# Kernel tuning notes

Measured on AMD Instinct MI355X. Metric: run time of the kernel, lower is better.

The kernel has to match this reference:

```python
import jax, jax.numpy as jnp
import numpy as np

B, T, O, N, M, H = 64, 128, 256, 65536, 64, 512
EPS = 1e-8


def setup_inputs() -> dict:
    key = jax.random.key(0)
    ks = jax.random.split(key, 8)
    x = jax.random.normal(ks[0], (B, T, O, 1), dtype=jnp.float32)
    # original: memory.uniform_(1e-05, 0.0001)
    memory0 = jax.random.uniform(ks[1], (N, M), dtype=jnp.float32, minval=1e-5, maxval=1e-4)
    eye = jnp.eye(B, N, dtype=jnp.float32)  # torch.eye(batch_size, N)
    h0 = jnp.zeros((B, H), dtype=jnp.float32)
    Wxh = jax.random.normal(ks[2], (O, H), dtype=jnp.float32) * 0.05
    Wrh = jax.random.normal(ks[3], (M, H), dtype=jnp.float32) * 0.1
    bh = jnp.zeros((H,), dtype=jnp.float32)
    Wo = jax.random.normal(ks[4], (H, O), dtype=jnp.float32) * 0.05
    bo = jnp.zeros((O,), dtype=jnp.float32)
    rW = jax.random.normal(ks[5], (H, M + 6), dtype=jnp.float32) * 0.05
    rb = jnp.zeros((M + 6,), dtype=jnp.float32)
    wW = jax.random.normal(ks[6], (H, 3 * M + 6), dtype=jnp.float32) * 0.05
    wb = jnp.zeros((3 * M + 6,), dtype=jnp.float32)
    return dict(x=x, memory0=memory0, wr=eye, ww=eye, h0=h0, Wxh=Wxh, Wrh=Wrh,
                bh=bh, Wo=Wo, bo=bo, rW=rW, rb=rb, wW=wW, wb=wb)


def _address(head_out, w_prev, mem):
    """Graves-2014 NTM addressing. head_out: (B, M+6) raw head projection."""
    k = jnp.tanh(head_out[:, :M])                          # key       (B, M)
    beta = jax.nn.softplus(head_out[:, M:M + 1])           # strength  (B, 1)
    g = jax.nn.sigmoid(head_out[:, M + 1:M + 2])           # gate      (B, 1)
    s = jax.nn.softmax(head_out[:, M + 2:M + 5], axis=-1)  # shift     (B, 3)
    gamma = 1.0 + jax.nn.softplus(head_out[:, M + 5:M + 6])  # sharpen (B, 1)
    kn = k / (jnp.linalg.norm(k, axis=-1, keepdims=True) + EPS)
    mn = mem / (jnp.linalg.norm(mem, axis=-1, keepdims=True) + EPS)
    wc = jax.nn.softmax(beta * (kn @ mn.T), axis=-1)       # content   (B, N)
    wg = g * wc + (1.0 - g) * w_prev                       # interpolate
    # circular shift conv over N with taps {-1, 0, +1}
    wt = (s[:, 0:1] * jnp.roll(wg, 1, axis=1)
          + s[:, 1:2] * wg
          + s[:, 2:3] * jnp.roll(wg, -1, axis=1))
    wp = (wt + EPS) ** gamma                               # sharpen
    return wp / jnp.sum(wp, axis=1, keepdims=True)


def reference(x, memory0, wr, ww, h0, Wxh, Wrh, bh, Wo, bo, rW, rb, wW, wb):
    xt = jnp.transpose(x, (1, 0, 2, 3)).reshape(T, B, O)  # time-major, flattened
    inv_b = 1.0 / B

    def step(carry, x_t):
        mem, h = carry
        # write head: address, then erase/add (memory shared across batch -> mean)
        wh = h @ wW + wb                                   # (B, 3M+6)
        w_w = _address(wh[:, :M + 6], ww, mem)             # (B, N)
        e = jax.nn.sigmoid(wh[:, M + 6:2 * M + 6])         # (B, M)
        a = jnp.tanh(wh[:, 2 * M + 6:3 * M + 6])           # (B, M)
        erase = jnp.einsum('bn,bm->nm', w_w, e) * inv_b    # (N, M)
        add = jnp.einsum('bn,bm->nm', w_w, a) * inv_b
        m_t = mem * (1.0 - erase) + add
        # read head
        rh = h @ rW + rb                                   # (B, M+6)
        w_r = _address(rh, wr, m_t)                        # (B, N)
        r_t = w_r @ m_t                                    # (B, M)
        # feedforward controller step + output
        h_new = jax.nn.relu(x_t @ Wxh + r_t @ Wrh + bh)    # (B, H)
        out = jax.nn.sigmoid(h_new @ Wo + bo)              # (B, O)
        return (m_t, h_new), out

    (_, _), outs = jax.lax.scan(step, (memory0, h0), xt)   # outs: (T, B, O)
    return jnp.transpose(outs, (1, 0, 2))                  # (B, T, O)
```

## Files before the change

### kernel.cpp

```cpp
#include <hip/hip_runtime.h>

#define NROWS 65536
#define BB 64
#define TT 128
#define OO 256
#define MM 64
#define HH 512
#define EPSF 1e-8f

__device__ __forceinline__ float wredsum(float v) {
#pragma unroll
  for (int o = 1; o < 64; o <<= 1) v += __shfl_xor(v, o, 64);
  return v;
}
__device__ __forceinline__ float sigm(float x) { return 1.f / (1.f + __expf(-x)); }
__device__ __forceinline__ float softplus_(float x) { return x > 20.f ? x : log1pf(__expf(x)); }

__global__ void __launch_bounds__(256) k_xpre(const float* __restrict__ x, const float* __restrict__ Wxh,
                                              const float* __restrict__ bh, float* __restrict__ Xpre) {
  __shared__ float xl[4][256];
  int tid = threadIdx.x;
#pragma unroll
  for (int i = 0; i < 4; ++i) {
    int pair = blockIdx.x * 4 + i;
    int t = pair >> 6, b = pair & 63;
    xl[i][tid] = x[((size_t)b * TT + t) * OO + tid];
  }
  __syncthreads();
  for (int u = 0; u < 2; ++u) {
    int hh = tid + u * 256;
    float a[4];
    float bv = bh[hh];
#pragma unroll
    for (int i = 0; i < 4; ++i) a[i] = bv;
    for (int o = 0; o < 256; ++o) {
      float wv = Wxh[(size_t)o * HH + hh];
#pragma unroll
      for (int i = 0; i < 4; ++i) a[i] += xl[i][o] * wv;
    }
#pragma unroll
    for (int i = 0; i < 4; ++i) {
      int pair = blockIdx.x * 4 + i;
      Xpre[(size_t)pair * HH + hh] = a[i];
    }
  }
}

__global__ void __launch_bounds__(256) k_w1(const float* __restrict__ msrc, const float* __restrict__ knwT,
                                            const float* __restrict__ prmw, float* __restrict__ E,
                                            float* __restrict__ Swst, float* __restrict__ S2rst) {
  int tid = threadIdx.x, blk = blockIdx.x;
  int base = blk * 64;
  __shared__ float rows[4096];
  __shared__ float sred[256];
  if (blk == 0) {
    for (int i = tid; i < 32 * 64; i += 256) S2rst[i] = 0.f;
  }
  {
    const float4* s4 = (const float4*)(msrc + (size_t)base * 64);
    float4* d4 = (float4*)rows;
#pragma unroll
    for (int i = 0; i < 4; ++i) d4[tid + i * 256] = s4[tid + i * 256];
  }
  int l = tid & 63, w = tid >> 6;
  float kr[64];
#pragma unroll
  for (int j = 0; j < 64; ++j) kr[j] = knwT[j * 64 + l];
  float beta = prmw[l * 8 + 0];
  __syncthreads();
  float sacc = 0.f;
  for (int r = w * 16; r < w * 16 + 16; ++r) {
    const float4* row4 = (const float4*)(rows + r * 64);
    float dot = 0.f, nsq = 0.f;
#pragma unroll
    for (int j = 0; j < 16; ++j) {
      float4 rv = row4[j];
      dot += kr[j * 4] * rv.x + kr[j * 4 + 1] * rv.y + kr[j * 4 + 2] * rv.z + kr[j * 4 + 3] * rv.w;
      nsq += rv.x * rv.x + rv.y * rv.y + rv.z * rv.z + rv.w * rv.w;
    }
    float ev = __expf(beta * dot / (sqrtf(nsq) + EPSF) - beta);
    E[(size_t)(base + r) * 64 + l] = ev;
    sacc += ev;
  }
  sred[tid] = sacc;
  __syncthreads();
  if (tid < 64)
    atomicAdd(&Swst[(blk & 31) * 64 + tid], sred[tid] + sred[tid + 64] + sred[tid + 128] + sred[tid + 192]);
}

__global__ void __launch_bounds__(256) k_w2(const float* __restrict__ E, const float* __restrict__ prmw,
                                            const float* __restrict__ Swst, float* __restrict__ wpg,
                                            float* __restrict__ S2wst) {
  int tid = threadIdx.x, blk = blockIdx.x, base = blk * 64;
  __shared__ float EL[66 * 64];
  __shared__ float Sw[64];
  __shared__ float sred[256];
  if (tid < 64) {
    float s = 0.f;
    for (int st = 0; st < 32; ++st) s += Swst[st * 64 + tid];
    Sw[tid] = s;
  }
  for (int i = tid; i < 66 * 64; i += 256) {
    int rr = i >> 6, b2 = i & 63;
    EL[i] = E[(size_t)((base - 1 + rr) & (NROWS - 1)) * 64 + b2];
  }
  __syncthreads();
  int b = tid & 63, w = tid >> 6;
  float g = prmw[b * 8 + 1], gam = prmw[b * 8 + 2];
  float s0 = prmw[b * 8 + 3], s1 = prmw[b * 8 + 4], s2 = prmw[b * 8 + 5];
  float gi = g / Sw[b], gm1 = 1.f - g;
  float s2acc = 0.f;
  for (int i = 0; i < 16; ++i) {
    int ln = w + i * 4;
    int n = base + ln;
    int nm = (n - 1) & (NROWS - 1), np = (n + 1) & (NROWS - 1);
    float wgm = gi * EL[ln * 64 + b] + (nm == b ? gm1 : 0.f);
    float wgc = gi * EL[(ln + 1) * 64 + b] + (n == b ? gm1 : 0.f);
    float wgp = gi * EL[(ln + 2) * 64 + b] + (np == b ? gm1 : 0.f);
    float wt = s0 * wgm + s1 * wgc + s2 * wgp;
    float wp = __powf(wt + EPSF, gam);
    wpg[(size_t)n * 64 + b] = wp;
    s2acc += wp;
  }
  sred[tid] = s2acc;
  __syncthreads();
  if (tid < 64)
    atomicAdd(&S2wst[(blk & 31) * 64 + tid], sred[tid] + sred[tid + 64] + sred[tid + 128] + sred[tid + 192]);
}

__global__ void __launch_bounds__(256) k_w3(const float* __restrict__ msrc, float* __restrict__ mdst,
                                            const float* __restrict__ wpg, const float* __restrict__ ea2,
                                            const float* __restrict__ knrT, const float* __restrict__ prmr,
                                            const float* __restrict__ S2wst, float* __restrict__ E,
                                            float* __restrict__ Srst) {
  int tid = threadIdx.x, blk = blockIdx.x, base = blk * 64;
  __shared__ float2 ealds[4096];
  __shared__ float wlT[4 * 64 * 20];
  __shared__ float fb[64];
  __shared__ float sred[256];
  {
    const float4* s4 = (const float4*)ea2;
    float4* d4 = (float4*)ealds;
#pragma unroll
    for (int i = 0; i < 8; ++i) d4[tid + i * 256] = s4[tid + i * 256];
  }
  if (tid < 64) {
    float s = 0.f;
    for (int st = 0; st < 32; ++st) s += S2wst[st * 64 + tid];
    fb[tid] = 1.f / (64.f * s);
  }
  __syncthreads();
  int l = tid & 63, w = tid >> 6;
#pragma unroll
  for (int k = 0; k < 16; ++k) {
    float wv = wpg[(size_t)(base + w * 16 + k) * 64 + l] * fb[l];
    wlT[(w * 64 + l) * 20 + k] = wv;
  }
  __syncthreads();
  float er[16], ad[16];
#pragma unroll
  for (int k = 0; k < 16; ++k) { er[k] = 0.f; ad[k] = 0.f; }
  for (int b2 = 0; b2 < 64; ++b2) {
    float2 eav = ealds[b2 * 64 + l];
    const float4* wrow = (const float4*)(wlT + (w * 64 + b2) * 20);
    float4 q0 = wrow[0], q1 = wrow[1], q2 = wrow[2], q3 = wrow[3];
    float qa[16];
    qa[0] = q0.x; qa[1] = q0.y; qa[2] = q0.z; qa[3] = q0.w;
    qa[4] = q1.x; qa[5] = q1.y; qa[6] = q1.z; qa[7] = q1.w;
    qa[8] = q2.x; qa[9] = q2.y; qa[10] = q2.z; qa[11] = q2.w;
    qa[12] = q3.x; qa[13] = q3.y; qa[14] = q3.z; qa[15] = q3.w;
#pragma unroll
    for (int k = 0; k < 16; ++k) { er[k] += qa[k] * eav.x; ad[k] += qa[k] * eav.y; }
  }
#pragma unroll
  for (int k = 0; k < 16; ++k) {
    int r = w * 16 + k;
    size_t n = (size_t)(base + r);
    float mv = msrc[n * 64 + l];
    mdst[n * 64 + l] = mv * (1.f - er[k]) + ad[k];
  }
  __syncthreads();
  float kr[64];
#pragma unroll
  for (int j = 0; j < 64; ++j) kr[j] = knrT[j * 64 + l];
  float beta_r = prmr[l * 8 + 0];
  float sacc = 0.f;
  for (int r = w * 16; r < w * 16 + 16; ++r) {
    const float4* row4 = (const float4*)(mdst + (size_t)(base + r) * 64);
    float dot = 0.f, nsq = 0.f;
#pragma unroll
    for (int j = 0; j < 16; ++j) {
      float4 rv = row4[j];
      dot += kr[j * 4] * rv.x + kr[j * 4 + 1] * rv.y + kr[j * 4 + 2] * rv.z + kr[j * 4 + 3] * rv.w;
      nsq += rv.x * rv.x + rv.y * rv.y + rv.z * rv.z + rv.w * rv.w;
    }
    float ev = __expf(beta_r * dot / (sqrtf(nsq) + EPSF) - beta_r);
    E[(size_t)(base + r) * 64 + l] = ev;
    sacc += ev;
  }
  sred[tid] = sacc;
  __syncthreads();
  if (tid < 64)
    atomicAdd(&Srst[(blk & 31) * 64 + tid], sred[tid] + sred[tid + 64] + sred[tid + 128] + sred[tid + 192]);
}

__global__ void __launch_bounds__(256) k_r2(const float* __restrict__ E, const float* __restrict__ mdst,
                                            const float* __restrict__ prmr, const float* __restrict__ Srst,
                                            float* __restrict__ part, float* __restrict__ S2rst) {
  int tid = threadIdx.x, blk = blockIdx.x, base = blk * 64;
  __shared__ float mt[4096];
  __shared__ float EL[66 * 64];
  __shared__ float Sr[64];
  __shared__ float sred[256];
  __shared__ float racc[64 * 65];
  if (tid < 64) {
    float s = 0.f;
    for (int st = 0; st < 32; ++st) s += Srst[st * 64 + tid];
    Sr[tid] = s;
  }
  {
    const float4* s4 = (const float4*)(mdst + (size_t)base * 64);
    float4* d4 = (float4*)mt;
#pragma unroll
    for (int i = 0; i < 4; ++i) d4[tid + i * 256] = s4[tid + i * 256];
  }
  for (int i = tid; i < 66 * 64; i += 256) {
    int rr = i >> 6, b2 = i & 63;
    EL[i] = E[(size_t)((base - 1 + rr) & (NROWS - 1)) * 64 + b2];
  }
  __syncthreads();
  int b = tid & 63, w = tid >> 6;
  float g = prmr[b * 8 + 1], gam = prmr[b * 8 + 2];
  float s0 = prmr[b * 8 + 3], s1 = prmr[b * 8 + 4], s2 = prmr[b * 8 + 5];
  float gi = g / Sr[b], gm1 = 1.f - g;
  float acc[64];
#pragma unroll
  for (int m = 0; m < 64; ++m) acc[m] = 0.f;
  float s2acc = 0.f;
  for (int i = 0; i < 16; ++i) {
    int r = w * 16 + i;
    int n = base + r;
    int nm = (n - 1) & (NROWS - 1), np = (n + 1) & (NROWS - 1);
    float wgm = gi * EL[r * 64 + b] + (nm == b ? gm1 : 0.f);
    float wgc = gi * EL[(r + 1) * 64 + b] + (n == b ? gm1 : 0.f);
    float wgp = gi * EL[(r + 2) * 64 + b] + (np == b ? gm1 : 0.f);
    float wt = s0 * wgm + s1 * wgc + s2 * wgp;
    float wp = __powf(wt + EPSF, gam);
    s2acc += wp;
    const float4* row4 = (const float4*)(mt + r * 64);
#pragma unroll
    for (int m4 = 0; m4 < 16; ++m4) {
      float4 mv = row4[m4];
      acc[m4 * 4 + 0] += wp * mv.x;
      acc[m4 * 4 + 1] += wp * mv.y;
      acc[m4 * 4 + 2] += wp * mv.z;
      acc[m4 * 4 + 3] += wp * mv.w;
    }
  }
  sred[tid] = s2acc;
  __syncthreads();
  if (tid < 64)
    atomicAdd(&S2rst[(blk & 31) * 64 + tid], sred[tid] + sred[tid + 64] + sred[tid + 128] + sred[tid + 192]);
  if (w == 0) {
#pragma unroll
    for (int m = 0; m < 64; ++m) racc[b * 65 + m] = acc[m];
  }
  __syncthreads();
  for (int ww2 = 1; ww2 < 4; ++ww2) {
    if (w == ww2) {
#pragma unroll
      for (int m = 0; m < 64; ++m) racc[b * 65 + m] += acc[m];
    }
    __syncthreads();
  }
  for (int i = tid; i < 4096; i += 256) part[(size_t)blk * 4096 + i] = racc[(i >> 6) * 65 + (i & 63)];
}

__global__ void __launch_bounds__(256) k_rr(const float* __restrict__ part, float* __restrict__ part2) {
  __shared__ float red[256];
  int rb = blockIdx.x;
  int b = rb >> 2, quarter = rb & 3;
  int tid = threadIdx.x;
  int m = tid & 63, pq = tid >> 6;
  float acc = 0.f;
  for (int p = quarter * 256 + pq; p < quarter * 256 + 256; p += 4)
    acc += part[((size_t)p * 64 + b) * 64 + m];
  red[tid] = acc;
  __syncthreads();
  if (tid < 64)
    part2[(size_t)rb * 64 + tid] = red[tid] + red[tid + 64] + red[tid + 128] + red[tid + 192];
}

__global__ void __launch_bounds__(512) k_cp(int t, const float* __restrict__ h0,
                                            const float* __restrict__ Xpre, float* __restrict__ Hbuf,
                                            const float* __restrict__ part2, const float* __restrict__ S2rst,
                                            const float* __restrict__ Wrh, const float* __restrict__ wW,
                                            const float* __restrict__ wb, const float* __restrict__ rW,
                                            const float* __restrict__ rb, float* __restrict__ knwT,
                                            float* __restrict__ knrT, float* __restrict__ ea2,
                                            float* __restrict__ prmw, float* __restrict__ prmr,
                                            float* __restrict__ zst) {
  int b = blockIdx.x, tid = threadIdx.x;
  __shared__ float hl[512];
  __shared__ float proj[268];
  __shared__ float red[512];
  __shared__ float rt[64];
  __shared__ float s2r_sh;
  if (t >= 0) {
    float v = 0.f;
    if (tid < 32) v = S2rst[tid * 64 + b];
    if (tid < 64) red[tid] = v;
    __syncthreads();
    if (tid == 0) {
      float s = 0.f;
      for (int i = 0; i < 32; ++i) s += red[i];
      s2r_sh = s;
    }
    __syncthreads();
    if (tid < 256) {
      int m = tid & 63, q = tid >> 6;
      red[tid] = part2[((size_t)b * 4 + q) * 64 + m];
    }
    __syncthreads();
    if (tid < 64) rt[tid] = (red[tid] + red[tid + 64] + red[tid + 128] + red[tid + 192]) / s2r_sh;
    __syncthreads();
    {
      int hh = tid;
      float a = Xpre[((size_t)t * 64 + b) * HH + hh];
      for (int m2 = 0; m2 < 64; ++m2) a += rt[m2] * Wrh[(size_t)m2 * HH + hh];
      a = fmaxf(a, 0.f);
      Hbuf[((size_t)t * 64 + b) * HH + hh] = a;
      hl[hh] = a;
    }
  } else {
    hl[tid] = h0[(size_t)b * HH + tid];
  }
  __syncthreads();
  if (b == 0) {
    for (int i = tid; i < 3 * 2048; i += 512) zst[i] = 0.f;
  }
  if (tid < 268) {
    int idx = tid;
    float a;
    if (idx < 198) {
      a = wb[idx];
      for (int hh = 0; hh < 512; ++hh) a += hl[hh] * wW[(size_t)hh * 198 + idx];
    } else {
      int jj = idx - 198;
      a = rb[jj];
      for (int hh = 0; hh < 512; ++hh) a += hl[hh] * rW[(size_t)hh * 70 + jj];
    }
    proj[idx] = a;
  }
  __syncthreads();
  int l = tid & 63, wv = tid >> 6;
  if (wv == 0) {
    float kv = tanhf(proj[l]);
    float s = wredsum(kv * kv);
    knwT[l * 64 + b] = kv / (sqrtf(s) + EPSF);
  } else if (wv == 1) {
    float kv = tanhf(proj[198 + l]);
    float s = wredsum(kv * kv);
    knrT[l * 64 + b] = kv / (sqrtf(s) + EPSF);
  } else if (wv == 2) {
    float ev = sigm(proj[70 + l]);
    float av = tanhf(proj[134 + l]);
    ((float2*)ea2)[b * 64 + l] = make_float2(ev, av);
  } else if (wv == 3) {
    if (l == 0) {
      float beta = softplus_(proj[64]);
      float g = sigm(proj[65]);
      float v0 = proj[66], v1 = proj[67], v2 = proj[68];
      float mx = fmaxf(v0, fmaxf(v1, v2));
      float e0 = __expf(v0 - mx), e1 = __expf(v1 - mx), e2 = __expf(v2 - mx);
      float is = 1.f / (e0 + e1 + e2);
      float gam = 1.f + softplus_(proj[69]);
      prmw[b * 8 + 0] = beta; prmw[b * 8 + 1] = g; prmw[b * 8 + 2] = gam;
      prmw[b * 8 + 3] = e0 * is; prmw[b * 8 + 4] = e1 * is; prmw[b * 8 + 5] = e2 * is;
    } else if (l == 1) {
      const int of = 198;
      float beta = softplus_(proj[of + 64]);
      float g = sigm(proj[of + 65]);
      float v0 = proj[of + 66], v1 = proj[of + 67], v2 = proj[of + 68];
      float mx = fmaxf(v0, fmaxf(v1, v2));
      float e0 = __expf(v0 - mx), e1 = __expf(v1 - mx), e2 = __expf(v2 - mx);
      float is = 1.f / (e0 + e1 + e2);
      float gam = 1.f + softplus_(proj[of + 69]);
      prmr[b * 8 + 0] = beta; prmr[b * 8 + 1] = g; prmr[b * 8 + 2] = gam;
      prmr[b * 8 + 3] = e0 * is; prmr[b * 8 + 4] = e1 * is; prmr[b * 8 + 5] = e2 * is;
    }
  }
}

__global__ void __launch_bounds__(256) k_out(const float* __restrict__ Hbuf, const float* __restrict__ Wo,
                                             const float* __restrict__ bo, float* __restrict__ out) {
  __shared__ float hl[4][512];
  int tid = threadIdx.x;
#pragma unroll
  for (int i = 0; i < 8; ++i) {
    int idx = tid + i * 256;
    hl[idx >> 9][idx & 511] = Hbuf[(size_t)blockIdx.x * 2048 + idx];
  }
  __syncthreads();
  float a[4];
  float bv = bo[tid];
#pragma unroll
  for (int i = 0; i < 4; ++i) a[i] = bv;
  for (int hh = 0; hh < 512; ++hh) {
    float wv = Wo[(size_t)hh * OO + tid];
#pragma unroll
    for (int i = 0; i < 4; ++i) a[i] += hl[i][hh] * wv;
  }
#pragma unroll
  for (int i = 0; i < 4; ++i) {
    int pair = blockIdx.x * 4 + i;
    int t = pair >> 6, b = pair & 63;
    out[((size_t)b * TT + t) * OO + tid] = 1.f / (1.f + __expf(-a[i]));
  }
}

extern "C" void kernel_launch(void* const* d_in, const int* in_sizes, int n_in,
                              void* d_out, int out_size, void* d_ws, size_t ws_size,
                              hipStream_t stream) {
  (void)in_sizes; (void)n_in; (void)out_size; (void)ws_size;
  const float* x    = (const float*)d_in[0];
  const float* mem0 = (const float*)d_in[1];
  const float* h0   = (const float*)d_in[4];
  const float* Wxh  = (const float*)d_in[5];
  const float* Wrh  = (const float*)d_in[6];
  const float* bh   = (const float*)d_in[7];
  const float* Wo   = (const float*)d_in[8];
  const float* bo   = (const float*)d_in[9];
  const float* rW   = (const float*)d_in[10];
  const float* rb   = (const float*)d_in[11];
  const float* wW   = (const float*)d_in[12];
  const float* wb   = (const float*)d_in[13];
  float* ws = (float*)d_ws;
  const size_t NM = (size_t)NROWS * MM;
  float* memA = ws;
  float* memB = memA + NM;
  float* E    = memB + NM;
  float* wpg  = E + NM;
  float* Xpre = wpg + NM;
  float* Hbuf = Xpre + NM;
  float* part = Hbuf + NM;
  float* part2 = part + NM;
  float* small = part2 + 16384;
  float* knwT = small;
  float* knrT = knwT + 4096;
  float* ea2  = knrT + 4096;
  float* prmw = ea2 + 8192;
  float* prmr = prmw + 512;
  float* Swst  = prmr + 512;
  float* S2wst = Swst + 2048;
  float* Srst  = S2wst + 2048;
  float* S2rst = Srst + 2048;

  hipMemcpyAsync(memA, mem0, NM * sizeof(float), hipMemcpyDeviceToDevice, stream);
  k_xpre<<<2048, 256, 0, stream>>>(x, Wxh, bh, Xpre);
  k_cp<<<64, 512, 0, stream>>>(-1, h0, Xpre, Hbuf, part2, S2rst, Wrh, wW, wb, rW, rb,
                               knwT, knrT, ea2, prmw, prmr, Swst);
  for (int t = 0; t < TT; ++t) {
    float* msrc = (t & 1) ? memB : memA;
    float* mdst = (t & 1) ? memA : memB;
    k_w1<<<1024, 256, 0, stream>>>(msrc, knwT, prmw, E, Swst, S2rst);
    k_w2<<<1024, 256, 0, stream>>>(E, prmw, Swst, wpg, S2wst);
    k_w3<<<1024, 256, 0, stream>>>(msrc, mdst, wpg, ea2, knrT, prmr, S2wst, E, Srst);
    k_r2<<<1024, 256, 0, stream>>>(E, mdst, prmr, Srst, part, S2rst);
    k_rr<<<256, 256, 0, stream>>>(part, part2);
    k_cp<<<64, 512, 0, stream>>>(t, h0, Xpre, Hbuf, part2, S2rst, Wrh, wW, wb, rW, rb,
                                 knwT, knrT, ea2, prmw, prmr, Swst);
  }
  k_out<<<2048, 256, 0, stream>>>(Hbuf, Wo, bo, (float*)d_out);
}
```

Measured before the change: 27.03 ms.

## Cache updated memory rows in LDS and fold partial read reduction into controller kernel

The write-update kernel stores each updated memory row in shared memory as well as global memory. The read-addressing similarity pass then reads from LDS instead of reloading from global. The separate partial-sum reduction kernel is removed, and the controller kernel now reduces all 1024 per-block partials itself, saving one launch per timestep and the intermediate buffer. The trade-off is a larger LDS footprint in k_w3 and a much larger serial reduction in the 64-block controller kernel.

```diff
diff --git a/kernel.cpp b/kernel.cpp
--- a/kernel.cpp
+++ b/kernel.cpp
@@ -136,6 +136,7 @@
   int tid = threadIdx.x, blk = blockIdx.x, base = blk * 64;
   __shared__ float2 ealds[4096];
   __shared__ float wlT[4 * 64 * 20];
+  __shared__ float rowsN[4096];
   __shared__ float fb[64];
   __shared__ float sred[256];
   {
@@ -177,7 +178,9 @@
     int r = w * 16 + k;
     size_t n = (size_t)(base + r);
     float mv = msrc[n * 64 + l];
-    mdst[n * 64 + l] = mv * (1.f - er[k]) + ad[k];
+    float nv = mv * (1.f - er[k]) + ad[k];
+    mdst[n * 64 + l] = nv;
+    rowsN[r * 64 + l] = nv;
   }
   __syncthreads();
   float kr[64];
@@ -186,7 +189,7 @@
   float beta_r = prmr[l * 8 + 0];
   float sacc = 0.f;
   for (int r = w * 16; r < w * 16 + 16; ++r) {
-    const float4* row4 = (const float4*)(mdst + (size_t)(base + r) * 64);
+    const float4* row4 = (const float4*)(rowsN + r * 64);
     float dot = 0.f, nsq = 0.f;
 #pragma unroll
     for (int j = 0; j < 16; ++j) {
@@ -276,24 +279,9 @@
   for (int i = tid; i < 4096; i += 256) part[(size_t)blk * 4096 + i] = racc[(i >> 6) * 65 + (i & 63)];
 }
 
-__global__ void __launch_bounds__(256) k_rr(const float* __restrict__ part, float* __restrict__ part2) {
-  __shared__ float red[256];
-  int rb = blockIdx.x;
-  int b = rb >> 2, quarter = rb & 3;
-  int tid = threadIdx.x;
-  int m = tid & 63, pq = tid >> 6;
-  float acc = 0.f;
-  for (int p = quarter * 256 + pq; p < quarter * 256 + 256; p += 4)
-    acc += part[((size_t)p * 64 + b) * 64 + m];
-  red[tid] = acc;
-  __syncthreads();
-  if (tid < 64)
-    part2[(size_t)rb * 64 + tid] = red[tid] + red[tid + 64] + red[tid + 128] + red[tid + 192];
-}
-
 __global__ void __launch_bounds__(512) k_cp(int t, const float* __restrict__ h0,
                                             const float* __restrict__ Xpre, float* __restrict__ Hbuf,
-                                            const float* __restrict__ part2, const float* __restrict__ S2rst,
+                                            const float* __restrict__ part, const float* __restrict__ S2rst,
                                             const float* __restrict__ Wrh, const float* __restrict__ wW,
                                             const float* __restrict__ wb, const float* __restrict__ rW,
                                             const float* __restrict__ rb, float* __restrict__ knwT,
@@ -317,12 +305,19 @@
       s2r_sh = s;
     }
     __syncthreads();
-    if (tid < 256) {
+    {
       int m = tid & 63, q = tid >> 6;
-      red[tid] = part2[((size_t)b * 4 + q) * 64 + m];
+      float acc = 0.f;
+      for (int p = q; p < 1024; p += 8) acc += part[((size_t)p * 64 + b) * 64 + m];
+      red[tid] = acc;
     }
     __syncthreads();
-    if (tid < 64) rt[tid] = (red[tid] + red[tid + 64] + red[tid + 128] + red[tid + 192]) / s2r_sh;
+    if (tid < 64) {
+      float r = 0.f;
+#pragma unroll
+      for (int q8 = 0; q8 < 8; ++q8) r += red[tid + q8 * 64];
+      rt[tid] = r / s2r_sh;
+    }
     __syncthreads();
     {
       int hh = tid;
@@ -444,8 +439,7 @@
   float* Xpre = wpg + NM;
   float* Hbuf = Xpre + NM;
   float* part = Hbuf + NM;
-  float* part2 = part + NM;
-  float* small = part2 + 16384;
+  float* small = part + NM;
   float* knwT = small;
   float* knrT = knwT + 4096;
   float* ea2  = knrT + 4096;
@@ -458,7 +452,7 @@
 
   hipMemcpyAsync(memA, mem0, NM * sizeof(float), hipMemcpyDeviceToDevice, stream);
   k_xpre<<<2048, 256, 0, stream>>>(x, Wxh, bh, Xpre);
-  k_cp<<<64, 512, 0, stream>>>(-1, h0, Xpre, Hbuf, part2, S2rst, Wrh, wW, wb, rW, rb,
+  k_cp<<<64, 512, 0, stream>>>(-1, h0, Xpre, Hbuf, part, S2rst, Wrh, wW, wb, rW, rb,
                                knwT, knrT, ea2, prmw, prmr, Swst);
   for (int t = 0; t < TT; ++t) {
     float* msrc = (t & 1) ? memB : memA;
@@ -467,8 +461,7 @@
     k_w2<<<1024, 256, 0, stream>>>(E, prmw, Swst, wpg, S2wst);
     k_w3<<<1024, 256, 0, stream>>>(msrc, mdst, wpg, ea2, knrT, prmr, S2wst, E, Srst);
     k_r2<<<1024, 256, 0, stream>>>(E, mdst, prmr, Srst, part, S2rst);
-    k_rr<<<256, 256, 0, stream>>>(part, part2);
-    k_cp<<<64, 512, 0, stream>>>(t, h0, Xpre, Hbuf, part2, S2rst, Wrh, wW, wb, rW, rb,
+    k_cp<<<64, 512, 0, stream>>>(t, h0, Xpre, Hbuf, part, S2rst, Wrh, wW, wb, rW, rb,
                                  knwT, knrT, ea2, prmw, prmr, Swst);
   }
   k_out<<<2048, 256, 0, stream>>>(Hbuf, Wo, bo, (float*)d_out);
```

After: 25.10 ms. 1.08x faster.
